# Optimization experiments

Hardware: AMD Instinct MI355X
Metric: run time of the kernel (lower is better)

Reference implementation:

```python
import jax, jax.numpy as jnp
import numpy as np

E = 8          # moe_num_experts
F = 4096       # ffn_hidden_size
D = 2048       # d_model
TOP_K = 2


def setup_inputs() -> dict:
    key = jax.random.key(0)
    k_x, k_r, k_w1, k_v1, k_w2 = jax.random.split(key, 5)
    scale = 0.02  # ~ normal initializer scale
    x = jax.random.normal(k_x, (2, 2048, D), dtype=jnp.float32)
    router_w = jax.random.normal(k_r, (D, E), dtype=jnp.float32) * scale
    w1 = jax.random.normal(k_w1, (E * F, D), dtype=jnp.float32) * scale
    v1 = jax.random.normal(k_v1, (E * F, D), dtype=jnp.float32) * scale
    w2 = jax.random.normal(k_w2, (E * F, D), dtype=jnp.float32) * scale
    return {"x": x, "router_w": router_w, "w1": w1, "v1": v1, "w2": w2}


def reference(x, router_w, w1, v1, w2):
    # --- Router: dense logits -> softmax (fp32) -> top-k -> L1 normalize ---
    logits = jnp.einsum("bsd,de->bse", x.astype(jnp.float32), router_w)
    weights = jax.nn.softmax(logits, axis=-1)                       # [B,S,E]
    top_weights, top_experts = jax.lax.top_k(weights, TOP_K)        # [B,S,K]
    # moe_normalize_expert_weights = 1 -> L1 norm
    top_weights = top_weights / jnp.sum(jnp.abs(top_weights), axis=-1, keepdims=True)
    top_weights = top_weights.astype(x.dtype)

    # --- Experts: dense per-expert GLU, masked combine (faithful to source) ---
    w1r = w1.reshape(E, F, D)
    v1r = v1.reshape(E, F, D)
    w2r = w2.reshape(E, F, D)
    out = jnp.zeros_like(x)
    for e in range(E):  # fixed small structural loop over experts
        x1 = jnp.einsum("bsd,fd->bsf", x, w1r[e])
        x2 = jnp.einsum("bsd,fd->bsf", x, v1r[e])
        h = jax.nn.silu(x1) * x2                                    # GLU
        y = jnp.einsum("bsf,fd->bsd", h, w2r[e])
        coef = jnp.sum((top_experts == e) * top_weights, axis=-1)[:, :, None]
        out = out + coef * y
    return out
```

## Files before the change

kernel.cpp:

```cpp
#include <hip/hip_runtime.h>
#include <cstdio>
#include <cstdint>

typedef _Float16 f16;
typedef _Float16 f16x8 __attribute__((ext_vector_type(8)));
typedef float f32x4 __attribute__((ext_vector_type(4)));

#define D_MODEL 2048
#define FFN     4096
#define FFN2    8192
#define NEXP    8
#define NTOK    4096
#define NENT    (NTOK*2)
#define BM      256
#define BN      256
#define BK      64
#define KSPLIT  4
#define KCHUNK  (FFN / KSPLIT)
#define MAX_ROWS  10240
#define MAX_TILES 40

__device__ __forceinline__ void gload_lds16(const void* g, void* l) {
  __builtin_amdgcn_global_load_lds(
      (const __attribute__((address_space(1))) void*)g,
      (__attribute__((address_space(3))) void*)l, 16, 0, 0);
}

template<int N> __device__ __forceinline__ void waitvm() {
  if constexpr (N == 0) asm volatile("s_waitcnt vmcnt(0)" ::: "memory");
  else if constexpr (N == 2) asm volatile("s_waitcnt vmcnt(2)" ::: "memory");
  else if constexpr (N == 4) asm volatile("s_waitcnt vmcnt(4)" ::: "memory");
  else if constexpr (N == 6) asm volatile("s_waitcnt vmcnt(6)" ::: "memory");
}

template<int LD>
__device__ __forceinline__ void stageA(const f16* aT, int k0, f16* AS, int mh, int tid) {
#pragma unroll
  for (int s = 0; s < 2; s++) {
    int o = s*8192 + tid*16;
    int rl = o >> 7;
    int ce = ((o & 127) ^ ((rl & 7) << 4)) >> 1;
    int arow = s*128 + mh*64 + (rl & 63);
    gload_lds16(aT + (size_t)arow * LD + k0 + ce,
                (char*)AS + mh*16384 + s*8192 + (tid & ~63)*16);
  }
}

template<int LD>
__device__ __forceinline__ void stageB(const f16* bT, int k0, f16* BS, int nh, int tid) {
#pragma unroll
  for (int s = 0; s < 2; s++) {
    int o = s*8192 + tid*16;
    int rl = o >> 7;
    int ce = ((o & 127) ^ ((rl & 7) << 4)) >> 1;
    int crow = (rl >> 5)*64 + nh*32 + (rl & 31);
    gload_lds16(bT + (size_t)crow * LD + k0 + ce,
                (char*)BS + nh*16384 + s*8192 + (tid & ~63)*16);
  }
}

__device__ __forceinline__ f16x8 fragLd(const f16* S, int row, int lane, int ks) {
  int kb = ks*64 + (lane >> 4)*16;
  int off = (row*128 + kb) ^ ((row & 7) << 4);
  return *(const f16x8*)((const char*)S + off);
}

template<int LD, int V0, int V1, int V3, bool SB0, bool SB1, bool SA1, bool SA0>
__device__ __forceinline__ void tile4(
    const f16* aT, const f16* bT, int k1, int k2,
    f16* ASc, f16* BSc, f16* ASn, f16* BSn,
    f32x4 (&acc)[8][4], f16x8 (&aF)[4][2], f16x8 (&bF)[2][2][2],
    int tid, int lane, int wrM, int wcN) {
#pragma unroll
  for (int mf = 0; mf < 4; mf++)
#pragma unroll
    for (int ks = 0; ks < 2; ks++)
      aF[mf][ks] = fragLd(ASc, wrM*64 + mf*16 + (lane & 15), lane, ks);
#pragma unroll
  for (int nf = 0; nf < 2; nf++)
#pragma unroll
    for (int ks = 0; ks < 2; ks++)
      bF[0][nf][ks] = fragLd(BSc, wcN*32 + nf*16 + (lane & 15), lane, ks);
  if constexpr (SB0) stageB<LD>(bT, k1, BSn, 0, tid);
  __builtin_amdgcn_s_barrier();
  __builtin_amdgcn_s_setprio(1);
#pragma unroll
  for (int mf = 0; mf < 4; mf++)
#pragma unroll
    for (int nf = 0; nf < 2; nf++)
#pragma unroll
      for (int ks = 0; ks < 2; ks++)
        acc[mf][nf] = __builtin_amdgcn_mfma_f32_16x16x32_f16(aF[mf][ks], bF[0][nf][ks], acc[mf][nf], 0, 0, 0);
  __builtin_amdgcn_s_setprio(0);
  waitvm<V0>();
  __builtin_amdgcn_s_barrier();
#pragma unroll
  for (int nf = 0; nf < 2; nf++)
#pragma unroll
    for (int ks = 0; ks < 2; ks++)
      bF[1][nf][ks] = fragLd(BSc, 128 + wcN*32 + nf*16 + (lane & 15), lane, ks);
  if constexpr (SB1) stageB<LD>(bT, k1, BSn, 1, tid);
  __builtin_amdgcn_s_barrier();
  __builtin_amdgcn_s_setprio(1);
#pragma unroll
  for (int mf = 0; mf < 4; mf++)
#pragma unroll
    for (int nf = 0; nf < 2; nf++)
#pragma unroll
      for (int ks = 0; ks < 2; ks++)
        acc[mf][2+nf] = __builtin_amdgcn_mfma_f32_16x16x32_f16(aF[mf][ks], bF[1][nf][ks], acc[mf][2+nf], 0, 0, 0);
  __builtin_amdgcn_s_setprio(0);
  waitvm<V1>();
  __builtin_amdgcn_s_barrier();
#pragma unroll
  for (int mf = 0; mf < 4; mf++)
#pragma unroll
    for (int ks = 0; ks < 2; ks++)
      aF[mf][ks] = fragLd(ASc, 128 + wrM*64 + mf*16 + (lane & 15), lane, ks);
  if constexpr (SA1) stageA<LD>(aT, k1, ASn, 1, tid);
  __builtin_amdgcn_s_barrier();
  __builtin_amdgcn_s_setprio(1);
#pragma unroll
  for (int mf = 0; mf < 4; mf++)
#pragma unroll
    for (int nf = 0; nf < 2; nf++)
#pragma unroll
      for (int ks = 0; ks < 2; ks++)
        acc[4+mf][nf] = __builtin_amdgcn_mfma_f32_16x16x32_f16(aF[mf][ks], bF[0][nf][ks], acc[4+mf][nf], 0, 0, 0);
  __builtin_amdgcn_s_setprio(0);
  __builtin_amdgcn_s_barrier();
  if constexpr (SA0) stageA<LD>(aT, k2, ASc, 0, tid);
  __builtin_amdgcn_s_barrier();
  __builtin_amdgcn_s_setprio(1);
#pragma unroll
  for (int mf = 0; mf < 4; mf++)
#pragma unroll
    for (int nf = 0; nf < 2; nf++)
#pragma unroll
      for (int ks = 0; ks < 2; ks++)
        acc[4+mf][2+nf] = __builtin_amdgcn_mfma_f32_16x16x32_f16(aF[mf][ks], bF[1][nf][ks], acc[4+mf][2+nf], 0, 0, 0);
  __builtin_amdgcn_s_setprio(0);
  waitvm<V3>();
  __builtin_amdgcn_s_barrier();
}


__global__ void zero_counts_kernel(int* counts) {
  if (threadIdx.x < NEXP) counts[threadIdx.x] = 0;
}

__global__ __launch_bounds__(64) void router_kernel(
    const float* __restrict__ x, const float* __restrict__ rw,
    int* counts, int* te, float* tw, int* trank) {
  int t = blockIdx.x;
  int lane = threadIdx.x;
  float acc[8] = {0.f,0.f,0.f,0.f,0.f,0.f,0.f,0.f};
  const float* xr = x + (size_t)t * D_MODEL;
  for (int d = lane; d < D_MODEL; d += 64) {
    float xv = xr[d];
    const float4* r4 = (const float4*)(rw + (size_t)d * NEXP);
    float4 a = r4[0], b = r4[1];
    acc[0] += xv*a.x; acc[1] += xv*a.y; acc[2] += xv*a.z; acc[3] += xv*a.w;
    acc[4] += xv*b.x; acc[5] += xv*b.y; acc[6] += xv*b.z; acc[7] += xv*b.w;
  }
#pragma unroll
  for (int off = 32; off > 0; off >>= 1) {
#pragma unroll
    for (int e = 0; e < 8; e++) acc[e] += __shfl_down(acc[e], off);
  }
  if (lane == 0) {
    int e0 = 0;
#pragma unroll
    for (int e = 1; e < 8; e++) if (acc[e] > acc[e0]) e0 = e;
    int e1 = (e0 == 0) ? 1 : 0;
#pragma unroll
    for (int e = 0; e < 8; e++) if (e != e0 && acc[e] > acc[e1]) e1 = e;
    float c0 = 1.0f / (1.0f + expf(acc[e1] - acc[e0]));
    float c1 = 1.0f - c0;
    int r0 = atomicAdd(&counts[e0], 1);
    int r1 = atomicAdd(&counts[e1], 1);
    te[t*2] = e0; te[t*2+1] = e1;
    tw[t*2] = c0; tw[t*2+1] = c1;
    trank[t*2] = r0; trank[t*2+1] = r1;
  }
}

__global__ void sched_kernel(const int* counts, int* offsets, int4* sched, int* nT) {
  if (threadIdx.x != 0 || blockIdx.x != 0) return;
  int off = 0, n = 0;
  for (int e = 0; e < NEXP; e++) {
    offsets[e] = off;
    int cnt = counts[e];
    int nt = (cnt + BM - 1) / BM;
    for (int i = 0; i < nt; i++) {
      sched[n] = make_int4(e, off + i*BM, min(BM, cnt - i*BM), 0);
      n++;
    }
    off += nt * BM;
  }
  offsets[NEXP] = off;
  *nT = n;
}

__global__ __launch_bounds__(256) void gather_kernel(
    const float* __restrict__ x, const int* __restrict__ te,
    const float* __restrict__ tw, const int* __restrict__ trank,
    const int* __restrict__ offsets, f16* __restrict__ xg,
    int* __restrict__ token_of, float* __restrict__ coefs) {
  int i = blockIdx.x;
  int t = i >> 1;
  int e = te[i];
  int slot = offsets[e] + trank[i];
  if (threadIdx.x == 0) { token_of[slot] = t; coefs[slot] = tw[i]; }
  const float4* src = (const float4*)(x + (size_t)t * D_MODEL);
  f16x8* dst = (f16x8*)(xg + (size_t)slot * D_MODEL);
  for (int j = threadIdx.x; j < D_MODEL/8; j += 256) {
    float4 v0 = src[j*2], v1 = src[j*2+1];
    f16x8 h;
    h[0]=(f16)v0.x; h[1]=(f16)v0.y; h[2]=(f16)v0.z; h[3]=(f16)v0.w;
    h[4]=(f16)v1.x; h[5]=(f16)v1.y; h[6]=(f16)v1.z; h[7]=(f16)v1.w;
    dst[j] = h;
  }
}

__global__ __launch_bounds__(256) void convert_both_kernel(
    const float* __restrict__ w1, const float* __restrict__ v1,
    f16* __restrict__ dst) {
  int n8 = NEXP*FFN*D_MODEL/8;
  int stride = gridDim.x * 256;
  for (int i = blockIdx.x*256 + threadIdx.x; i < n8; i += stride) {
    int d8 = i & (D_MODEL/8 - 1);
    int fr_glob = i >> 8;
    int e = fr_glob >> 12;
    int fr = fr_glob & (FFN - 1);
    int crbase = ((fr >> 4)*2)*16 + (fr & 15);
    float4 a0 = ((const float4*)w1)[(size_t)i*2];
    float4 a1 = ((const float4*)w1)[(size_t)i*2 + 1];
    float4 b0 = ((const float4*)v1)[(size_t)i*2];
    float4 b1 = ((const float4*)v1)[(size_t)i*2 + 1];
    f16x8 ha, hb;
    ha[0]=(f16)a0.x; ha[1]=(f16)a0.y; ha[2]=(f16)a0.z; ha[3]=(f16)a0.w;
    ha[4]=(f16)a1.x; ha[5]=(f16)a1.y; ha[6]=(f16)a1.z; ha[7]=(f16)a1.w;
    hb[0]=(f16)b0.x; hb[1]=(f16)b0.y; hb[2]=(f16)b0.z; hb[3]=(f16)b0.w;
    hb[4]=(f16)b1.x; hb[5]=(f16)b1.y; hb[6]=(f16)b1.z; hb[7]=(f16)b1.w;
    size_t base = ((size_t)e*FFN2 + crbase)*(D_MODEL/8) + d8;
    ((f16x8*)dst)[base] = ha;
    ((f16x8*)dst)[base + 16*(D_MODEL/8)] = hb;
  }
}

__global__ __launch_bounds__(256) void transpose_w2_kernel(
    const float* __restrict__ w2, f16* __restrict__ w2t) {
  __shared__ float tl[64][65];
  int e = blockIdx.z;
  int d0 = blockIdx.x * 64, f0 = blockIdx.y * 64;
  const float* src = w2 + (size_t)e * FFN * D_MODEL;
  int tid = threadIdx.x;
  int fr = tid >> 4, c4 = (tid & 15) * 4;
#pragma unroll
  for (int rr = 0; rr < 4; rr++) {
    float4 v = *(const float4*)(src + (size_t)(f0 + fr + rr*16) * D_MODEL + d0 + c4);
    tl[fr + rr*16][c4+0] = v.x; tl[fr + rr*16][c4+1] = v.y;
    tl[fr + rr*16][c4+2] = v.z; tl[fr + rr*16][c4+3] = v.w;
  }
  __syncthreads();
  int dr = tid >> 2, fg = (tid & 3) * 16;
  f16* dst = w2t + (size_t)e * D_MODEL * FFN + (size_t)(d0 + dr) * FFN + f0 + fg;
  f16 tmp[16];
#pragma unroll
  for (int j = 0; j < 16; j++) tmp[j] = (f16)tl[fg + j][dr];
  *(float4*)(dst)     = *(float4*)(tmp);
  *(float4*)(dst + 8) = *(float4*)(tmp + 8);
}

__global__ __launch_bounds__(512, 2) void phaseA_kernel(
    const f16* __restrict__ xg, const f16* __restrict__ w12h,
    f16* __restrict__ hbuf, const int4* __restrict__ sched, const int* __restrict__ nT) {
  int nwg = gridDim.x * gridDim.y;
  int flat = blockIdx.x + gridDim.x * blockIdx.y;
  int q = nwg >> 3, r = nwg & 7;
  int xcd = flat & 7, loc = flat >> 3;
  int swz = (xcd < r ? xcd*(q+1) : r*(q+1) + (xcd-r)*q) + loc;
  int tile = swz >> 5;
  if (tile >= *nT) return;
  int fc0 = (swz & 31) * BN;
  int4 sc = sched[tile];
  int e = sc.x, row0 = sc.y;

  __shared__ f16 AS[2][BM*BK];
  __shared__ f16 BS[2][BN*BK];

  int tid = threadIdx.x, lane = tid & 63, wid = tid >> 6;
  int wrM = wid >> 2, wcN = wid & 3;

  const f16* aT = xg  + (size_t)row0 * D_MODEL;
  const f16* bT = w12h + (size_t)e * FFN2 * D_MODEL + (size_t)fc0 * D_MODEL;

  f32x4 acc[8][4]; f16x8 aF[4][2]; f16x8 bF[2][2][2];
  f32x4 z4 = {0.f,0.f,0.f,0.f};
#pragma unroll
  for (int m = 0; m < 8; m++)
#pragma unroll
    for (int n = 0; n < 4; n++) acc[m][n] = z4;

  stageA<D_MODEL>(aT, 0, AS[0], 0, tid);
  stageB<D_MODEL>(bT, 0, BS[0], 0, tid);
  stageB<D_MODEL>(bT, 0, BS[0], 1, tid);
  stageA<D_MODEL>(aT, 0, AS[0], 1, tid);
  stageA<D_MODEL>(aT, BK, AS[1], 0, tid);
  waitvm<6>();
  __builtin_amdgcn_s_barrier();

  constexpr int NTILES = D_MODEL / BK;
  for (int t = 0; t + 2 < NTILES; t++) {
    int b = t & 1;
    tile4<D_MODEL,6,6,6,true,true,true,true>(aT, bT, (t+1)*BK, (t+2)*BK,
        AS[b], BS[b], AS[b^1], BS[b^1], acc, aF, bF, tid, lane, wrM, wcN);
  }
  { int b = (NTILES-2) & 1;
    tile4<D_MODEL,6,6,4,true,true,true,false>(aT, bT, (NTILES-1)*BK, 0,
        AS[b], BS[b], AS[b^1], BS[b^1], acc, aF, bF, tid, lane, wrM, wcN); }
  { int b = (NTILES-1) & 1;
    tile4<D_MODEL,2,0,-1,false,false,false,false>(aT, bT, 0, 0,
        AS[b], BS[b], AS[b^1], BS[b^1], acc, aF, bF, tid, lane, wrM, wcN); }

  int i15 = lane & 15, l4 = lane >> 4;
#pragma unroll
  for (int m = 0; m < 8; m++) {
    int rowl = wrM*128 + (m>>2)*64 + (m&3)*16 + l4*4;
#pragma unroll
    for (int nh = 0; nh < 2; nh++) {
      int f = (fc0 >> 1) + wcN*32 + nh*16 + i15;
      f16* hb = hbuf + (size_t)(row0 + rowl) * FFN + f;
#pragma unroll
      for (int q2 = 0; q2 < 4; q2++) {
        float x1 = acc[m][nh*2+0][q2], x2 = acc[m][nh*2+1][q2];
        float hv = x1 / (1.0f + __expf(-x1)) * x2;
        hb[(size_t)q2 * FFN] = (f16)hv;
      }
    }
  }
}

__global__ __launch_bounds__(512, 2) void phaseB_kernel(
    const f16* __restrict__ hbuf, const f16* __restrict__ w2t,
    f16* __restrict__ yb0, f16* __restrict__ ybR,
    const int4* __restrict__ sched, const int* __restrict__ nT) {
  int nwg = gridDim.x * gridDim.y * gridDim.z;
  int flat = blockIdx.x + gridDim.x * (blockIdx.y + gridDim.y * blockIdx.z);
  int q = nwg >> 3, r = nwg & 7;
  int xcd = flat & 7, loc = flat >> 3;
  int swz = (xcd < r ? xcd*(q+1) : r*(q+1) + (xcd-r)*q) + loc;
  int z = swz / (MAX_TILES * 8);
  int rem = swz - z * (MAX_TILES * 8);
  int tile = rem >> 3;
  if (tile >= *nT) return;
  int dc0 = (rem & 7) * BN;
  int4 sc = sched[tile];
  int e = sc.x, row0 = sc.y;

  __shared__ f16 AS[2][BM*BK];
  __shared__ f16 BS[2][BN*BK];

  int tid = threadIdx.x, lane = tid & 63, wid = tid >> 6;
  int wrM = wid >> 2, wcN = wid & 3;

  const f16* aT = hbuf + (size_t)row0 * FFN + z * KCHUNK;
  const f16* bT = w2t + (size_t)e * D_MODEL * FFN + (size_t)dc0 * FFN + z * KCHUNK;

  f32x4 acc[8][4]; f16x8 aF[4][2]; f16x8 bF[2][2][2];
  f32x4 z4 = {0.f,0.f,0.f,0.f};
#pragma unroll
  for (int m = 0; m < 8; m++)
#pragma unroll
    for (int n = 0; n < 4; n++) acc[m][n] = z4;

  stageA<FFN>(aT, 0, AS[0], 0, tid);
  stageB<FFN>(bT, 0, BS[0], 0, tid);
  stageB<FFN>(bT, 0, BS[0], 1, tid);
  stageA<FFN>(aT, 0, AS[0], 1, tid);
  stageA<FFN>(aT, BK, AS[1], 0, tid);
  waitvm<6>();
  __builtin_amdgcn_s_barrier();

  constexpr int NTILES = KCHUNK / BK;
  for (int t = 0; t + 2 < NTILES; t++) {
    int b = t & 1;
    tile4<FFN,6,6,6,true,true,true,true>(aT, bT, (t+1)*BK, (t+2)*BK,
        AS[b], BS[b], AS[b^1], BS[b^1], acc, aF, bF, tid, lane, wrM, wcN);
  }
  { int b = (NTILES-2) & 1;
    tile4<FFN,6,6,4,true,true,true,false>(aT, bT, (NTILES-1)*BK, 0,
        AS[b], BS[b], AS[b^1], BS[b^1], acc, aF, bF, tid, lane, wrM, wcN); }
  { int b = (NTILES-1) & 1;
    tile4<FFN,2,0,-1,false,false,false,false>(aT, bT, 0, 0,
        AS[b], BS[b], AS[b^1], BS[b^1], acc, aF, bF, tid, lane, wrM, wcN); }

  f16* yb = (z == 0) ? yb0 : (ybR + (size_t)(z-1) * MAX_ROWS * D_MODEL);
  int i15 = lane & 15, l4 = lane >> 4;
#pragma unroll
  for (int m = 0; m < 8; m++) {
#pragma unroll
    for (int q2 = 0; q2 < 4; q2++) {
      int rl = wrM*128 + (m>>2)*64 + (m&3)*16 + l4*4 + q2;
      f16* yrow = yb + (size_t)(row0 + rl) * D_MODEL + dc0 + wcN*64;
#pragma unroll
      for (int n = 0; n < 4; n++)
        yrow[(n>>1)*32 + (n&1)*16 + i15] = (f16)acc[m][n][q2];
    }
  }
}

__global__ __launch_bounds__(256) void combine_kernel(
    const f16* __restrict__ yb0, const f16* __restrict__ ybR,
    const int* __restrict__ te, const float* __restrict__ tw,
    const int* __restrict__ trank, const int* __restrict__ offsets,
    float* __restrict__ out) {
  int t = blockIdx.x;
  int d8 = threadIdx.x;
  int s0 = offsets[te[2*t]]   + trank[2*t];
  int s1 = offsets[te[2*t+1]] + trank[2*t+1];
  float w0 = tw[2*t], w1 = tw[2*t+1];
  float sum[8] = {0.f,0.f,0.f,0.f,0.f,0.f,0.f,0.f};
#pragma unroll
  for (int z = 0; z < KSPLIT; z++) {
    const f16* yb = (z == 0) ? yb0 : (ybR + (size_t)(z-1) * MAX_ROWS * D_MODEL);
    f16x8 a = ((const f16x8*)(yb + (size_t)s0 * D_MODEL))[d8];
    f16x8 b = ((const f16x8*)(yb + (size_t)s1 * D_MODEL))[d8];
#pragma unroll
    for (int j = 0; j < 8; j++) sum[j] += w0 * (float)a[j] + w1 * (float)b[j];
  }
  float* o = out + (size_t)t * D_MODEL + d8*8;
  float4 o0 = {sum[0], sum[1], sum[2], sum[3]};
  float4 o1 = {sum[4], sum[5], sum[6], sum[7]};
  ((float4*)o)[0] = o0;
  ((float4*)o)[1] = o1;
}

extern "C" void kernel_launch(void* const* d_in, const int* in_sizes, int n_in,
                              void* d_out, int out_size, void* d_ws, size_t ws_size,
                              hipStream_t stream) {
  const float* x  = (const float*)d_in[0];
  const float* rw = (const float*)d_in[1];
  const float* w1 = (const float*)d_in[2];
  const float* v1 = (const float*)d_in[3];
  const float* w2 = (const float*)d_in[4];
  float* out = (float*)d_out;

  char* p = (char*)d_ws;
  auto alloc = [&](size_t bytes) {
    char* r = p;
    p += (bytes + 255) & ~(size_t)255;
    return r;
  };
  int*   counts   = (int*)  alloc(NEXP * 4);
  int*   nT       = (int*)  alloc(4);
  int*   offsets  = (int*)  alloc((NEXP + 1) * 4);
  int*   te       = (int*)  alloc(NENT * 4);
  float* tw       = (float*)alloc(NENT * 4);
  int*   trank    = (int*)  alloc(NENT * 4);
  int*   token_of = (int*)  alloc(MAX_ROWS * 4);
  float* coefs    = (float*)alloc(MAX_ROWS * 4);
  int4*  sched    = (int4*) alloc(MAX_TILES * 16);
  f16*   xg       = (f16*)  alloc((size_t)MAX_ROWS * D_MODEL * 2);
  f16*   hbuf     = (f16*)  alloc((size_t)MAX_ROWS * FFN * 2);
  f16*   w12h     = (f16*)  alloc((size_t)NEXP * FFN2 * D_MODEL * 2);
  f16*   w2t      = (f16*)  alloc((size_t)NEXP * FFN * D_MODEL * 2);
  size_t needed = (size_t)(p - (char*)d_ws);
  if (needed > ws_size) {
    fprintf(stderr, "kernel_launch: ws too small: need %zu, have %zu\n", needed, ws_size);
    return;
  }
  f16* yb0 = xg;
  f16* ybR = w12h;

  zero_counts_kernel<<<1, 64, 0, stream>>>(counts);
  router_kernel<<<NTOK, 64, 0, stream>>>(x, rw, counts, te, tw, trank);
  sched_kernel<<<1, 1, 0, stream>>>(counts, offsets, sched, nT);
  gather_kernel<<<NENT, 256, 0, stream>>>(x, te, tw, trank, offsets, xg, token_of, coefs);
  convert_both_kernel<<<4096, 256, 0, stream>>>(w1, v1, w12h);
  transpose_w2_kernel<<<dim3(D_MODEL/64, FFN/64, NEXP), 256, 0, stream>>>(w2, w2t);
  phaseA_kernel<<<dim3(FFN2/BN, MAX_TILES), 512, 0, stream>>>(xg, w12h, hbuf, sched, nT);
  phaseB_kernel<<<dim3(D_MODEL/BN, MAX_TILES, KSPLIT), 512, 0, stream>>>(hbuf, w2t, yb0, ybR, sched, nT);
  combine_kernel<<<NTOK, 256, 0, stream>>>(yb0, ybR, te, tw, trank, offsets, out);
}
```

Baseline: 958.4 us.

## Replace fine-grained interleaved GEMM pipeline with simple double-buffered K loop

```diff
diff --git a/kernel.cpp b/kernel.cpp
--- a/kernel.cpp
+++ b/kernel.cpp
@@ -26,11 +26,8 @@
       (__attribute__((address_space(3))) void*)l, 16, 0, 0);
 }
 
-template<int N> __device__ __forceinline__ void waitvm() {
-  if constexpr (N == 0) asm volatile("s_waitcnt vmcnt(0)" ::: "memory");
-  else if constexpr (N == 2) asm volatile("s_waitcnt vmcnt(2)" ::: "memory");
-  else if constexpr (N == 4) asm volatile("s_waitcnt vmcnt(4)" ::: "memory");
-  else if constexpr (N == 6) asm volatile("s_waitcnt vmcnt(6)" ::: "memory");
+__device__ __forceinline__ void waitvm0() {
+  asm volatile("s_waitcnt vmcnt(0)" ::: "memory");
 }
 
 template<int LD>
@@ -65,82 +62,54 @@
   return *(const f16x8*)((const char*)S + off);
 }
 
-template<int LD, int V0, int V1, int V3, bool SB0, bool SB1, bool SA1, bool SA0>
-__device__ __forceinline__ void tile4(
-    const f16* aT, const f16* bT, int k1, int k2,
-    f16* ASc, f16* BSc, f16* ASn, f16* BSn,
-    f32x4 (&acc)[8][4], f16x8 (&aF)[4][2], f16x8 (&bF)[2][2][2],
-    int tid, int lane, int wrM, int wcN) {
+__device__ __forceinline__ void quad(
+    f32x4 (&acc)[8][4], int mo, int no,
+    f16x8 (&aF)[4][2], f16x8 (&bFh)[2][2]) {
 #pragma unroll
   for (int mf = 0; mf < 4; mf++)
 #pragma unroll
+    for (int nf = 0; nf < 2; nf++)
+#pragma unroll
+      for (int ks = 0; ks < 2; ks++)
+        acc[mo+mf][no+nf] = __builtin_amdgcn_mfma_f32_16x16x32_f16(
+            aF[mf][ks], bFh[nf][ks], acc[mo+mf][no+nf], 0, 0, 0);
+}
+
+template<int LD, bool STG>
+__device__ __forceinline__ void tileK2(
+    const f16* aT, const f16* bT, int k1,
+    const f16* ASc, const f16* BSc, f16* ASn, f16* BSn,
+    f32x4 (&acc)[8][4], int tid, int lane, int wrM, int wcN) {
+  if constexpr (STG) {
+    stageA<LD>(aT, k1, ASn, 0, tid);
+    stageA<LD>(aT, k1, ASn, 1, tid);
+    stageB<LD>(bT, k1, BSn, 0, tid);
+    stageB<LD>(bT, k1, BSn, 1, tid);
+  }
+  f16x8 aF[4][2], bF[2][2][2];
+  int i15 = lane & 15;
+#pragma unroll
+  for (int mf = 0; mf < 4; mf++)
+#pragma unroll
     for (int ks = 0; ks < 2; ks++)
-      aF[mf][ks] = fragLd(ASc, wrM*64 + mf*16 + (lane & 15), lane, ks);
-#pragma unroll
-  for (int nf = 0; nf < 2; nf++)
+      aF[mf][ks] = fragLd(ASc, wrM*64 + mf*16 + i15, lane, ks);
+#pragma unroll
+  for (int h = 0; h < 2; h++)
+#pragma unroll
+    for (int nf = 0; nf < 2; nf++)
+#pragma unroll
+      for (int ks = 0; ks < 2; ks++)
+        bF[h][nf][ks] = fragLd(BSc, h*128 + wcN*32 + nf*16 + i15, lane, ks);
+  quad(acc, 0, 0, aF, bF[0]);
+  quad(acc, 0, 2, aF, bF[1]);
+#pragma unroll
+  for (int mf = 0; mf < 4; mf++)
 #pragma unroll
     for (int ks = 0; ks < 2; ks++)
-      bF[0][nf][ks] = fragLd(BSc, wcN*32 + nf*16 + (lane & 15), lane, ks);
-  if constexpr (SB0) stageB<LD>(bT, k1, BSn, 0, tid);
-  __builtin_amdgcn_s_barrier();
-  __builtin_amdgcn_s_setprio(1);
-#pragma unroll
-  for (int mf = 0; mf < 4; mf++)
-#pragma unroll
-    for (int nf = 0; nf < 2; nf++)
-#pragma unroll
-      for (int ks = 0; ks < 2; ks++)
-        acc[mf][nf] = __builtin_amdgcn_mfma_f32_16x16x32_f16(aF[mf][ks], bF[0][nf][ks], acc[mf][nf], 0, 0, 0);
-  __builtin_amdgcn_s_setprio(0);
-  waitvm<V0>();
-  __builtin_amdgcn_s_barrier();
-#pragma unroll
-  for (int nf = 0; nf < 2; nf++)
-#pragma unroll
-    for (int ks = 0; ks < 2; ks++)
-      bF[1][nf][ks] = fragLd(BSc, 128 + wcN*32 + nf*16 + (lane & 15), lane, ks);
-  if constexpr (SB1) stageB<LD>(bT, k1, BSn, 1, tid);
-  __builtin_amdgcn_s_barrier();
-  __builtin_amdgcn_s_setprio(1);
-#pragma unroll
-  for (int mf = 0; mf < 4; mf++)
-#pragma unroll
-    for (int nf = 0; nf < 2; nf++)
-#pragma unroll
-      for (int ks = 0; ks < 2; ks++)
-        acc[mf][2+nf] = __builtin_amdgcn_mfma_f32_16x16x32_f16(aF[mf][ks], bF[1][nf][ks], acc[mf][2+nf], 0, 0, 0);
-  __builtin_amdgcn_s_setprio(0);
-  waitvm<V1>();
-  __builtin_amdgcn_s_barrier();
-#pragma unroll
-  for (int mf = 0; mf < 4; mf++)
-#pragma unroll
-    for (int ks = 0; ks < 2; ks++)
-      aF[mf][ks] = fragLd(ASc, 128 + wrM*64 + mf*16 + (lane & 15), lane, ks);
-  if constexpr (SA1) stageA<LD>(aT, k1, ASn, 1, tid);
-  __builtin_amdgcn_s_barrier();
-  __builtin_amdgcn_s_setprio(1);
-#pragma unroll
-  for (int mf = 0; mf < 4; mf++)
-#pragma unroll
-    for (int nf = 0; nf < 2; nf++)
-#pragma unroll
-      for (int ks = 0; ks < 2; ks++)
-        acc[4+mf][nf] = __builtin_amdgcn_mfma_f32_16x16x32_f16(aF[mf][ks], bF[0][nf][ks], acc[4+mf][nf], 0, 0, 0);
-  __builtin_amdgcn_s_setprio(0);
-  __builtin_amdgcn_s_barrier();
-  if constexpr (SA0) stageA<LD>(aT, k2, ASc, 0, tid);
-  __builtin_amdgcn_s_barrier();
-  __builtin_amdgcn_s_setprio(1);
-#pragma unroll
-  for (int mf = 0; mf < 4; mf++)
-#pragma unroll
-    for (int nf = 0; nf < 2; nf++)
-#pragma unroll
-      for (int ks = 0; ks < 2; ks++)
-        acc[4+mf][2+nf] = __builtin_amdgcn_mfma_f32_16x16x32_f16(aF[mf][ks], bF[1][nf][ks], acc[4+mf][2+nf], 0, 0, 0);
-  __builtin_amdgcn_s_setprio(0);
-  waitvm<V3>();
+      aF[mf][ks] = fragLd(ASc, 128 + wrM*64 + mf*16 + i15, lane, ks);
+  quad(acc, 4, 0, aF, bF[0]);
+  quad(acc, 4, 2, aF, bF[1]);
+  if constexpr (STG) waitvm0();
   __builtin_amdgcn_s_barrier();
 }
 
@@ -276,16 +245,11 @@
 __global__ __launch_bounds__(512, 2) void phaseA_kernel(
     const f16* __restrict__ xg, const f16* __restrict__ w12h,
     f16* __restrict__ hbuf, const int4* __restrict__ sched, const int* __restrict__ nT) {
-  int nwg = gridDim.x * gridDim.y;
-  int flat = blockIdx.x + gridDim.x * blockIdx.y;
-  int q = nwg >> 3, r = nwg & 7;
-  int xcd = flat & 7, loc = flat >> 3;
-  int swz = (xcd < r ? xcd*(q+1) : r*(q+1) + (xcd-r)*q) + loc;
-  int tile = swz >> 5;
+  int tile = blockIdx.y;
   if (tile >= *nT) return;
-  int fc0 = (swz & 31) * BN;
   int4 sc = sched[tile];
   int e = sc.x, row0 = sc.y;
+  int fc0 = blockIdx.x * BN;
 
   __shared__ f16 AS[2][BM*BK];
   __shared__ f16 BS[2][BN*BK];
@@ -296,7 +260,7 @@
   const f16* aT = xg  + (size_t)row0 * D_MODEL;
   const f16* bT = w12h + (size_t)e * FFN2 * D_MODEL + (size_t)fc0 * D_MODEL;
 
-  f32x4 acc[8][4]; f16x8 aF[4][2]; f16x8 bF[2][2][2];
+  f32x4 acc[8][4];
   f32x4 z4 = {0.f,0.f,0.f,0.f};
 #pragma unroll
   for (int m = 0; m < 8; m++)
@@ -304,25 +268,20 @@
     for (int n = 0; n < 4; n++) acc[m][n] = z4;
 
   stageA<D_MODEL>(aT, 0, AS[0], 0, tid);
+  stageA<D_MODEL>(aT, 0, AS[0], 1, tid);
   stageB<D_MODEL>(bT, 0, BS[0], 0, tid);
   stageB<D_MODEL>(bT, 0, BS[0], 1, tid);
-  stageA<D_MODEL>(aT, 0, AS[0], 1, tid);
-  stageA<D_MODEL>(aT, BK, AS[1], 0, tid);
-  waitvm<6>();
+  waitvm0();
   __builtin_amdgcn_s_barrier();
 
   constexpr int NTILES = D_MODEL / BK;
-  for (int t = 0; t + 2 < NTILES; t++) {
+  for (int t = 0; t < NTILES - 1; t++) {
     int b = t & 1;
-    tile4<D_MODEL,6,6,6,true,true,true,true>(aT, bT, (t+1)*BK, (t+2)*BK,
-        AS[b], BS[b], AS[b^1], BS[b^1], acc, aF, bF, tid, lane, wrM, wcN);
-  }
-  { int b = (NTILES-2) & 1;
-    tile4<D_MODEL,6,6,4,true,true,true,false>(aT, bT, (NTILES-1)*BK, 0,
-        AS[b], BS[b], AS[b^1], BS[b^1], acc, aF, bF, tid, lane, wrM, wcN); }
-  { int b = (NTILES-1) & 1;
-    tile4<D_MODEL,2,0,-1,false,false,false,false>(aT, bT, 0, 0,
-        AS[b], BS[b], AS[b^1], BS[b^1], acc, aF, bF, tid, lane, wrM, wcN); }
+    tileK2<D_MODEL,true>(aT, bT, (t+1)*BK, AS[b], BS[b], AS[b^1], BS[b^1],
+                         acc, tid, lane, wrM, wcN);
+  }
+  tileK2<D_MODEL,false>(aT, bT, 0, AS[(NTILES-1)&1], BS[(NTILES-1)&1],
+                        AS[NTILES&1], BS[NTILES&1], acc, tid, lane, wrM, wcN);
 
   int i15 = lane & 15, l4 = lane >> 4;
 #pragma unroll
@@ -346,18 +305,12 @@
     const f16* __restrict__ hbuf, const f16* __restrict__ w2t,
     f16* __restrict__ yb0, f16* __restrict__ ybR,
     const int4* __restrict__ sched, const int* __restrict__ nT) {
-  int nwg = gridDim.x * gridDim.y * gridDim.z;
-  int flat = blockIdx.x + gridDim.x * (blockIdx.y + gridDim.y * blockIdx.z);
-  int q = nwg >> 3, r = nwg & 7;
-  int xcd = flat & 7, loc = flat >> 3;
-  int swz = (xcd < r ? xcd*(q+1) : r*(q+1) + (xcd-r)*q) + loc;
-  int z = swz / (MAX_TILES * 8);
-  int rem = swz - z * (MAX_TILES * 8);
-  int tile = rem >> 3;
+  int tile = blockIdx.y;
   if (tile >= *nT) return;
-  int dc0 = (rem & 7) * BN;
   int4 sc = sched[tile];
   int e = sc.x, row0 = sc.y;
+  int dc0 = blockIdx.x * BN;
+  int z = blockIdx.z;
 
   __shared__ f16 AS[2][BM*BK];
   __shared__ f16 BS[2][BN*BK];
@@ -368,7 +321,7 @@
   const f16* aT = hbuf + (size_t)row0 * FFN + z * KCHUNK;
   const f16* bT = w2t + (size_t)e * D_MODEL * FFN + (size_t)dc0 * FFN + z * KCHUNK;
 
-  f32x4 acc[8][4]; f16x8 aF[4][2]; f16x8 bF[2][2][2];
+  f32x4 acc[8][4];
   f32x4 z4 = {0.f,0.f,0.f,0.f};
 #pragma unroll
   for (int m = 0; m < 8; m++)
@@ -376,25 +329,20 @@
     for (int n = 0; n < 4; n++) acc[m][n] = z4;
 
   stageA<FFN>(aT, 0, AS[0], 0, tid);
+  stageA<FFN>(aT, 0, AS[0], 1, tid);
   stageB<FFN>(bT, 0, BS[0], 0, tid);
   stageB<FFN>(bT, 0, BS[0], 1, tid);
-  stageA<FFN>(aT, 0, AS[0], 1, tid);
-  stageA<FFN>(aT, BK, AS[1], 0, tid);
-  waitvm<6>();
+  waitvm0();
   __builtin_amdgcn_s_barrier();
 
   constexpr int NTILES = KCHUNK / BK;
-  for (int t = 0; t + 2 < NTILES; t++) {
+  for (int t = 0; t < NTILES - 1; t++) {
     int b = t & 1;
-    tile4<FFN,6,6,6,true,true,true,true>(aT, bT, (t+1)*BK, (t+2)*BK,
-        AS[b], BS[b], AS[b^1], BS[b^1], acc, aF, bF, tid, lane, wrM, wcN);
-  }
-  { int b = (NTILES-2) & 1;
-    tile4<FFN,6,6,4,true,true,true,false>(aT, bT, (NTILES-1)*BK, 0,
-        AS[b], BS[b], AS[b^1], BS[b^1], acc, aF, bF, tid, lane, wrM, wcN); }
-  { int b = (NTILES-1) & 1;
-    tile4<FFN,2,0,-1,false,false,false,false>(aT, bT, 0, 0,
-        AS[b], BS[b], AS[b^1], BS[b^1], acc, aF, bF, tid, lane, wrM, wcN); }
+    tileK2<FFN,true>(aT, bT, (t+1)*BK, AS[b], BS[b], AS[b^1], BS[b^1],
+                     acc, tid, lane, wrM, wcN);
+  }
+  tileK2<FFN,false>(aT, bT, 0, AS[(NTILES-1)&1], BS[(NTILES-1)&1],
+                    AS[NTILES&1], BS[NTILES&1], acc, tid, lane, wrM, wcN);
 
   f16* yb = (z == 0) ? yb0 : (ybR + (size_t)(z-1) * MAX_ROWS * D_MODEL);
   int i15 = lane & 15, l4 = lane >> 4;
```

Result: slower. 1.009 ms (+5.3%).
